# Optimization experiments

Hardware: AMD Instinct MI355X
Metric: run time of the kernel (lower is better)

The kernel has to match this reference:

```python
import jax, jax.numpy as jnp
import numpy as np

N, M = 65536, 512
CTRL = 128
IN_DIM = 128
READ_LEN = M + 6          # [M,1,1,3,1]
WRITE_LEN = 3 * M + 6     # [M,1,1,3,1,M,M]
EPS = 1e-16


def setup_inputs() -> dict:
    key = jax.random.key(0)
    ks = jax.random.split(key, 12)
    s = 0.02
    return {
        "x":   jax.random.normal(ks[0], (4, IN_DIM), jnp.float32),
        "mem": jax.random.normal(ks[1], (N, M), jnp.float32) * 0.05,
        "Wc":  jax.random.normal(ks[2], (CTRL, IN_DIM), jnp.float32) * s,
        "bc":  jnp.zeros((CTRL,), jnp.float32),
        "Wr":  jax.random.normal(ks[3], (READ_LEN, CTRL), jnp.float32) * s,
        "br":  jnp.zeros((READ_LEN,), jnp.float32),
        "Ww":  jax.random.normal(ks[4], (WRITE_LEN, CTRL), jnp.float32) * s,
        "bw":  jnp.zeros((WRITE_LEN,), jnp.float32),
        "W1":  jax.random.normal(ks[5], (200, M + CTRL), jnp.float32) * s,
        "b1":  jnp.zeros((200,), jnp.float32),
        "W2":  jax.random.normal(ks[6], (10, 200), jnp.float32) * s,
        "b2":  jnp.zeros((10,), jnp.float32),
    }


def _address(mem, k, beta, g, s, gamma, w_prev):
    # content + gate + circular shift + sharpen (standard NTM addressing)
    beta = jax.nn.softplus(beta)
    g = jax.nn.sigmoid(g)
    s = jax.nn.softmax(s)                      # (3,)
    gamma = 1.0 + jax.nn.softplus(gamma)
    # cosine similarity against all N memory rows
    dot = mem @ k                              # (N,)
    norms = jnp.sqrt(jnp.sum(mem * mem, axis=1)) * jnp.sqrt(jnp.sum(k * k)) + EPS
    wc = jax.nn.softmax(beta * dot / norms)    # content weights (N,)
    wg = g * wc + (1.0 - g) * w_prev           # gated
    # circular convolution with 3-tap shift kernel s = [s(-1), s(0), s(+1)]
    ws = s[0] * jnp.roll(wg, 1) + s[1] * wg + s[2] * jnp.roll(wg, -1)
    w = ws ** gamma                            # sharpen
    return w / (jnp.sum(w) + EPS)


def _forward(x, mem, Wc, bc, Wr, br, Ww, bw, W1, b1, W2, b2):
    cont = x @ Wc.T + bc                       # controller: (4, 128)
    w0 = jnp.full((N,), 1.0 / N, x.dtype)      # softmax of constant -> uniform

    def step(carry, c_t):
        mem, w_r, w_w = carry
        # ---- write head ----
        ow = c_t @ Ww.T + bw                   # (3M+6,)
        k, b, g, s, y = ow[:M], ow[M], ow[M+1], ow[M+2:M+5], ow[M+5]
        e, a = ow[M+6:2*M+6], ow[2*M+6:]
        w_w = _address(mem, k, b, g, s, y, w_w)
        e = jax.nn.sigmoid(e)
        mem = mem * (1.0 - jnp.outer(w_w, e)) + jnp.outer(w_w, a)
        # ---- read head ----
        orr = c_t @ Wr.T + br                  # (M+6,)
        k, b, g, s, y = orr[:M], orr[M], orr[M+1], orr[M+2:M+5], orr[M+5]
        w_r = _address(mem, k, b, g, s, y, w_r)
        r = w_r @ mem                          # (M,)
        # ---- output MLP ----
        h = jax.nn.relu(jnp.concatenate([c_t, r]) @ W1.T + b1)
        out = h @ W2.T + b2                    # (10,)
        return (mem, w_r, w_w), out

    _, outs = jax.lax.scan(step, (mem, w0, w0), cont)
    return outs                                # (4, 10)


def reference(x, mem, Wc, bc, Wr, br, Ww, bw, W1, b1, W2, b2):
    return _forward(x, mem, Wc, bc, Wr, br, Ww, bw, W1, b1, W2, b2)
```

## Files before the change

### kernel.cpp

```cpp
#include <hip/hip_runtime.h>
#include <hip/hip_cooperative_groups.h>
#include <hip/hip_fp16.h>
#include <math.h>

namespace cg = cooperative_groups;

#define NN    65536
#define CTRLD 128
#define WLEN  1542
#define RLEN  518
#define EPSF  1e-16f
#define GRIDB 1024
#define ROWSB 64
#define RPWV  16

struct KP {
  const float* mem0; const float* cont;
  float* mem16;
  const float* kW; const float* sW; const float* eW; const float* aW;
  const float* kR; const float* sR; float* kn;
  float *dotR, *dotW, *n2v;
  float *wunW, *pSW, *wunR, *pSR;
  float *pZr, *pZw;
  float *rp, *p2, *hbuf;
  const float *W1, *b1, *W2, *b2;
  float* out;
  const float *x, *Wc, *bc, *Ww, *bw, *Wr, *br;
  float *contw, *kWw, *sWw, *eWw, *aWw, *kRw, *sRw;
};

struct Smem { float red[256]; float big[2048]; float zsh[4][2]; };

__device__ __forceinline__ float softplusf_(float x){
    return x > 0.f ? x + log1pf(expf(-x)) : log1pf(expf(x));
}
__device__ __forceinline__ float sigmoidf_(float x){ return 1.f/(1.f+expf(-x)); }
__device__ __forceinline__ float dot4_(const float4& a, const float4& b){
    return a.x*b.x + a.y*b.y + a.z*b.z + a.w*b.w;
}

__device__ __forceinline__ float blockReduce256(float v, float* red){
    int t = threadIdx.x;
    red[t] = v; __syncthreads();
    for(int s = 128; s; s >>= 1){ if(t < s) red[t] += red[t+s]; __syncthreads(); }
    float r = red[0]; __syncthreads();
    return r;
}
__device__ __forceinline__ void waveReduce3(float& a, float& b, float& c){
    for(int o = 32; o; o >>= 1){
        a += __shfl_down(a,o); b += __shfl_down(b,o); c += __shfl_down(c,o);
    }
}
__device__ __forceinline__ void waveReduce1(float& a){
    for(int o = 32; o; o >>= 1) a += __shfl_down(a,o);
}

__device__ __forceinline__ void owor_phase(const KP& p, Smem& sm, int bid){
    float* cs = sm.big;
    int tid = threadIdx.x;
    for(int q = tid; q < 512; q += 256){
        int t = q >> 7, c = q & 127;
        float acc = p.bc[c];
        const float* xr = p.x + t*CTRLD;
        const float* wr = p.Wc + c*CTRLD;
        for(int d = 0; d < CTRLD; ++d) acc += xr[d]*wr[d];
        cs[q] = acc;
        if(bid == 0) p.contw[q] = acc;
    }
    __syncthreads();
    int idx = bid*256 + tid;
    if(idx < 4*WLEN){
        int t = idx / WLEN, o = idx % WLEN;
        float acc = p.bw[o];
        const float* cr = cs + t*CTRLD;
        const float* wr = p.Ww + o*CTRLD;
        for(int d = 0; d < CTRLD; ++d) acc += cr[d]*wr[d];
        if(o < 512)       p.kWw[t*512 + o] = acc;
        else if(o < 518)  p.sWw[t*8 + (o-512)] = acc;
        else if(o < 1030) p.eWw[t*512 + (o-518)] = sigmoidf_(acc);
        else              p.aWw[t*512 + (o-1030)] = acc;
    } else {
        int j = idx - 4*WLEN;
        if(j < 4*RLEN){
            int t = j / RLEN, o = j % RLEN;
            float acc = p.br[o];
            const float* cr = cs + t*CTRLD;
            const float* wr = p.Wr + o*CTRLD;
            for(int d = 0; d < CTRLD; ++d) acc += cr[d]*wr[d];
            if(o < 512) p.kRw[t*512 + o] = acc;
            else        p.sRw[t*8 + (o-512)] = acc;
        }
    }
    __syncthreads();
}

template<int CH, bool RP, bool UPD, bool DOTR, bool DOTW, bool CVT>
__device__ __forceinline__ void sweep_phase(const KP& p, Smem& sm, int rstep,
    const float* kRc, const float* sRc, int knRi,
    const float* kWn, const float* sWn, int knWi)
{
    constexpr int NW = CH + (UPD ? 1 : 0);
    constexpr int NA = (NW > 0) ? NW : 1;
    int t = threadIdx.x, bid = blockIdx.x;
    float wnorm[NA];
    #pragma unroll
    for(int j = 0; j < NW; ++j){
        float s = p.pSW[j*GRIDB+t] + p.pSW[j*GRIDB+t+256]
                + p.pSW[j*GRIDB+t+512] + p.pSW[j*GRIDB+t+768];
        wnorm[j] = 1.f/(blockReduce256(s, sm.red) + EPSF);
    }
    int wave = t >> 6, lane = t & 63;
    int c0 = 2*lane, c1 = 2*lane + 1;
    float4 ev0[NA], ev1[NA], av0[NA], av1[NA];
    #pragma unroll
    for(int j = 0; j < NW; ++j){
        ev0[j] = ((const float4*)(p.eW + j*512))[c0];
        ev1[j] = ((const float4*)(p.eW + j*512))[c1];
        av0[j] = ((const float4*)(p.aW + j*512))[c0];
        av1[j] = ((const float4*)(p.aW + j*512))[c1];
    }
    float4 kra, krb, kwa, kwb;
    float betaR = 0.f, betaW = 0.f, knRv = 1.f, knWv = 1.f;
    if constexpr(DOTR){
        kra = ((const float4*)kRc)[c0]; krb = ((const float4*)kRc)[c1];
        betaR = softplusf_(sRc[0]);
        float n2 = blockReduce256(dot4_(kra,kra) + dot4_(krb,krb), sm.red);
        knRv = sqrtf(n2*0.25f);
        if(t == 0 && bid == 0) p.kn[knRi] = knRv;
    }
    if constexpr(DOTW){
        kwa = ((const float4*)kWn)[c0]; kwb = ((const float4*)kWn)[c1];
        betaW = softplusf_(sWn[0]);
        float n2 = blockReduce256(dot4_(kwa,kwa) + dot4_(kwb,kwb), sm.red);
        knWv = sqrtf(n2*0.25f);
        if(t == 0 && bid == 0) p.kn[knWi] = knWv;
    }
    float4 rpA = {0,0,0,0}, rpB = {0,0,0,0};
    float zr = 0.f, zw = 0.f;
    int row0 = bid*ROWSB + wave*RPWV;
    for(int r = 0; r < RPWV; ++r){
        int row = row0 + r;
        float4 v0, v1;
        if constexpr(CVT){
            const float4* src = (const float4*)p.mem0;
            v0 = src[(size_t)row*128 + c0];
            v1 = src[(size_t)row*128 + c1];
        } else {
            float4 raw = ((const float4*)p.mem16)[(size_t)row*64 + lane];
            const __half2* hp = (const __half2*)&raw;
            float2 f0 = __half22float2(hp[0]);
            float2 f1 = __half22float2(hp[1]);
            float2 f2 = __half22float2(hp[2]);
            float2 f3 = __half22float2(hp[3]);
            v0 = make_float4(f0.x, f0.y, f1.x, f1.y);
            v1 = make_float4(f2.x, f2.y, f3.x, f3.y);
        }
        #pragma unroll
        for(int j = 0; j < CH; ++j){
            float w = p.wunW[(size_t)j*NN + row]*wnorm[j];
            v0.x = fmaf(w, fmaf(-ev0[j].x, v0.x, av0[j].x), v0.x);
            v0.y = fmaf(w, fmaf(-ev0[j].y, v0.y, av0[j].y), v0.y);
            v0.z = fmaf(w, fmaf(-ev0[j].z, v0.z, av0[j].z), v0.z);
            v0.w = fmaf(w, fmaf(-ev0[j].w, v0.w, av0[j].w), v0.w);
            v1.x = fmaf(w, fmaf(-ev1[j].x, v1.x, av1[j].x), v1.x);
            v1.y = fmaf(w, fmaf(-ev1[j].y, v1.y, av1[j].y), v1.y);
            v1.z = fmaf(w, fmaf(-ev1[j].z, v1.z, av1[j].z), v1.z);
            v1.w = fmaf(w, fmaf(-ev1[j].w, v1.w, av1[j].w), v1.w);
        }
        if constexpr(RP){
            float wr = p.wunR[(size_t)rstep*NN + row];
            rpA.x += wr*v0.x; rpA.y += wr*v0.y; rpA.z += wr*v0.z; rpA.w += wr*v0.w;
            rpB.x += wr*v1.x; rpB.y += wr*v1.y; rpB.z += wr*v1.z; rpB.w += wr*v1.w;
        }
        if constexpr(UPD){
            float w = p.wunW[(size_t)CH*NN + row]*wnorm[CH];
            v0.x = fmaf(w, fmaf(-ev0[CH].x, v0.x, av0[CH].x), v0.x);
            v0.y = fmaf(w, fmaf(-ev0[CH].y, v0.y, av0[CH].y), v0.y);
            v0.z = fmaf(w, fmaf(-ev0[CH].z, v0.z, av0[CH].z), v0.z);
            v0.w = fmaf(w, fmaf(-ev0[CH].w, v0.w, av0[CH].w), v0.w);
            v1.x = fmaf(w, fmaf(-ev1[CH].x, v1.x, av1[CH].x), v1.x);
            v1.y = fmaf(w, fmaf(-ev1[CH].y, v1.y, av1[CH].y), v1.y);
            v1.z = fmaf(w, fmaf(-ev1[CH].z, v1.z, av1[CH].z), v1.z);
            v1.w = fmaf(w, fmaf(-ev1[CH].w, v1.w, av1[CH].w), v1.w);
        }
        if constexpr(CVT){
            float4 packed;
            __half2* op = (__half2*)&packed;
            op[0] = __floats2half2_rn(v0.x, v0.y);
            op[1] = __floats2half2_rn(v0.z, v0.w);
            op[2] = __floats2half2_rn(v1.x, v1.y);
            op[3] = __floats2half2_rn(v1.z, v1.w);
            ((float4*)p.mem16)[(size_t)row*64 + lane] = packed;
        }
        if constexpr(DOTR || DOTW){
            float d = 0.f, dn = 0.f;
            float n = dot4_(v0,v0) + dot4_(v1,v1);
            if constexpr(DOTR) d  = dot4_(v0,kra) + dot4_(v1,krb);
            if constexpr(DOTW) dn = dot4_(v0,kwa) + dot4_(v1,kwb);
            waveReduce3(d, dn, n);
            if(lane == 0){
                p.n2v[row] = n;
                float sn = sqrtf(n);
                if constexpr(DOTR){ p.dotR[row] = d;  zr += expf(betaR*d /(sn*knRv + EPSF)); }
                if constexpr(DOTW){ p.dotW[row] = dn; zw += expf(betaW*dn/(sn*knWv + EPSF)); }
            }
        }
    }
    if constexpr(DOTR || DOTW){
        if(lane == 0){ sm.zsh[wave][0] = zr; sm.zsh[wave][1] = zw; }
    }
    if constexpr(RP){
        ((float4*)(sm.big + wave*512))[c0] = rpA;
        ((float4*)(sm.big + wave*512))[c1] = rpB;
    }
    __syncthreads();
    if constexpr(RP){
        p.rp[(size_t)bid*512 + t] =
            sm.big[t] + sm.big[512+t] + sm.big[1024+t] + sm.big[1536+t];
        p.rp[(size_t)bid*512 + t + 256] =
            sm.big[t+256] + sm.big[768+t] + sm.big[1280+t] + sm.big[1792+t];
    }
    if(t == 0){
        if constexpr(DOTR) p.pZr[bid] = sm.zsh[0][0]+sm.zsh[1][0]+sm.zsh[2][0]+sm.zsh[3][0];
        if constexpr(DOTW) p.pZw[bid] = sm.zsh[0][1]+sm.zsh[1][1]+sm.zsh[2][1]+sm.zsh[3][1];
    }
    __syncthreads();
}

__device__ __forceinline__ void whead_phase(const KP& p, Smem& sm,
    const float* sV, const float* dotv, const float* pZ,
    const float* wprev, const float* pSprev, int knidx,
    float* wun, float* pSout)
{
    int t = threadIdx.x, bid = blockIdx.x;
    float z = pZ[t] + pZ[t+256] + pZ[t+512] + pZ[t+768];
    float Z = blockReduce256(z, sm.red);
    float invSp = 1.f;
    if(pSprev){
        float sp = pSprev[t] + pSprev[t+256] + pSprev[t+512] + pSprev[t+768];
        invSp = 1.f/(blockReduce256(sp, sm.red) + EPSF);
    }
    float beta  = softplusf_(sV[0]);
    float g     = sigmoidf_(sV[1]);
    float s0 = sV[2], s1 = sV[3], s2 = sV[4];
    float smx = fmaxf(s0, fmaxf(s1, s2));
    float e0 = expf(s0-smx), e1 = expf(s1-smx), e2 = expf(s2-smx);
    float es = e0+e1+e2;
    s0 = e0/es; s1 = e1/es; s2 = e2/es;
    float gamma = 1.f + softplusf_(sV[5]);
    float knv = p.kn[knidx];
    float invZ = 1.f/Z;
    float wu = 0.f;
    if(t < ROWSB){
        int i = bid*ROWSB + t;
        int im = (i-1) & (NN-1), ip = (i+1) & (NN-1);
        auto wgf = [&](int j)->float{
            float a = beta*dotv[j]/(sqrtf(p.n2v[j])*knv + EPSF);
            float pv = wprev ? wprev[j]*invSp : (1.f/NN);
            return g*expf(a)*invZ + (1.f-g)*pv;
        };
        wu = powf(s0*wgf(im) + s1*wgf(i) + s2*wgf(ip), gamma);
        wun[i] = wu;
    }
    float S = blockReduce256(wu, sm.red);
    if(t == 0) pSout[bid] = S;
}

__device__ __forceinline__ void rsum1_phase(const KP& p, float* dst){
    int t = threadIdx.x, b = blockIdx.x;
    float2 acc; acc.x = 0.f; acc.y = 0.f;
    const float2* r2 = (const float2*)p.rp;
    for(int j = 0; j < 16; ++j){
        float2 v = r2[(size_t)(b*16 + j)*256 + t];
        acc.x += v.x; acc.y += v.y;
    }
    ((float2*)dst)[b*256 + t] = acc;
}

__device__ __forceinline__ void h_phase(const KP& p, Smem& sm, int hb, int step,
                                        const float* p2src){
    int t = threadIdx.x;
    const float* pS = p.pSR + step*GRIDB;
    float sp = pS[t] + pS[t+256] + pS[t+512] + pS[t+768];
    float invS = 1.f/(blockReduce256(sp, sm.red) + EPSF);
    float2 acc; acc.x = 0.f; acc.y = 0.f;
    const float2* q = (const float2*)p2src;
    for(int j = 0; j < 64; ++j){
        float2 v = q[j*256 + t];
        acc.x += v.x; acc.y += v.y;
    }
    float* conc = sm.big;
    conc[128 + 2*t]     = acc.x*invS;
    conc[128 + 2*t + 1] = acc.y*invS;
    if(t < 128) conc[t] = p.cont[step*128 + t];
    __syncthreads();
    int wave = t >> 6, lane = t & 63;
    for(int ol = wave; ol < 25; ol += 4){
        int o = hb*25 + ol;
        const float* wr = p.W1 + (size_t)o*640;
        float a = 0.f;
        for(int q2 = lane; q2 < 640; q2 += 64) a += wr[q2]*conc[q2];
        waveReduce1(a);
        if(lane == 0) p.hbuf[step*200 + o] = fmaxf(a + p.b1[o], 0.f);
    }
    __syncthreads();
}

__device__ __forceinline__ void out_phase(const KP& p, int step){
    int t = threadIdx.x;
    if(t < 10){
        float a = p.b2[t];
        const float* wr = p.W2 + t*200;
        const float* h = p.hbuf + step*200;
        for(int j = 0; j < 200; ++j) a += wr[j]*h[j];
        p.out[step*10 + t] = a;
    }
}

__device__ __forceinline__ void hfull_phase(const KP& p, Smem& sm, int step,
                                            const float* p2src){
    int t = threadIdx.x;
    const float* pS = p.pSR + step*GRIDB;
    float sp = pS[t] + pS[t+256] + pS[t+512] + pS[t+768];
    float invS = 1.f/(blockReduce256(sp, sm.red) + EPSF);
    float2 acc; acc.x = 0.f; acc.y = 0.f;
    const float2* q = (const float2*)p2src;
    for(int j = 0; j < 64; ++j){
        float2 v = q[j*256 + t];
        acc.x += v.x; acc.y += v.y;
    }
    float* conc = sm.big;
    conc[128 + 2*t]     = acc.x*invS;
    conc[128 + 2*t + 1] = acc.y*invS;
    if(t < 128) conc[t] = p.cont[step*128 + t];
    __syncthreads();
    int wave = t >> 6, lane = t & 63;
    float* hsh = sm.big + 1024;
    for(int o = wave; o < 200; o += 4){
        const float* wr = p.W1 + (size_t)o*640;
        float a = 0.f;
        for(int q2 = lane; q2 < 640; q2 += 64) a += wr[q2]*conc[q2];
        waveReduce1(a);
        if(lane == 0) hsh[o] = fmaxf(a + p.b1[o], 0.f);
    }
    __syncthreads();
    if(t < 10){
        float a = p.b2[t];
        const float* wr = p.W2 + t*200;
        for(int j = 0; j < 200; ++j) a += wr[j]*hsh[j];
        p.out[step*10 + t] = a;
    }
}

__global__ void __launch_bounds__(256, 4) k_coop(KP p){
    cg::grid_group g = cg::this_grid();
    __shared__ Smem sm;
    int bid = blockIdx.x;
    if(bid < 33) owor_phase(p, sm, bid);
    g.sync();
    sweep_phase<0,false,false,false,true,true>(p, sm, 0, nullptr,nullptr,0, p.kW, p.sW, 0);
    g.sync();
    whead_phase(p, sm, p.sW, p.dotW, p.pZw, nullptr, nullptr, 0, p.wunW, p.pSW);
    g.sync();
    sweep_phase<0,false,true,true,true,false>(p, sm, 0, p.kR, p.sR, 1, p.kW+512, p.sW+8, 2);
    g.sync();
    whead_phase(p, sm, p.sR, p.dotR, p.pZr, nullptr, nullptr, 1, p.wunR, p.pSR);
    whead_phase(p, sm, p.sW+8, p.dotW, p.pZw, p.wunW, p.pSW, 2, p.wunW+NN, p.pSW+GRIDB);
    g.sync();
    sweep_phase<1,true,true,true,true,false>(p, sm, 0, p.kR+512, p.sR+8, 3, p.kW+1024, p.sW+16, 4);
    g.sync();
    whead_phase(p, sm, p.sR+8, p.dotR, p.pZr, p.wunR, p.pSR, 3, p.wunR+NN, p.pSR+GRIDB);
    whead_phase(p, sm, p.sW+16, p.dotW, p.pZw, p.wunW+NN, p.pSW+GRIDB, 4,
                p.wunW+2*(size_t)NN, p.pSW+2*GRIDB);
    if(bid < 64) rsum1_phase(p, p.p2);
    g.sync();
    sweep_phase<2,true,true,true,true,false>(p, sm, 1, p.kR+1024, p.sR+16, 5, p.kW+1536, p.sW+24, 6);
    g.sync();
    whead_phase(p, sm, p.sR+16, p.dotR, p.pZr, p.wunR+NN, p.pSR+GRIDB, 5,
                p.wunR+2*(size_t)NN, p.pSR+2*GRIDB);
    whead_phase(p, sm, p.sW+24, p.dotW, p.pZw, p.wunW+2*(size_t)NN, p.pSW+2*GRIDB, 6,
                p.wunW+3*(size_t)NN, p.pSW+3*GRIDB);
    if(bid < 64) rsum1_phase(p, p.p2 + 64*512);
    if(bid >= 64 && bid < 72) h_phase(p, sm, bid-64, 0, p.p2);
    g.sync();
    sweep_phase<3,true,true,true,false,false>(p, sm, 2, p.kR+1536, p.sR+24, 7, nullptr,nullptr,0);
    g.sync();
    whead_phase(p, sm, p.sR+24, p.dotR, p.pZr, p.wunR+2*(size_t)NN, p.pSR+2*GRIDB, 7,
                p.wunR+3*(size_t)NN, p.pSR+3*GRIDB);
    if(bid < 64) rsum1_phase(p, p.p2);
    if(bid >= 64 && bid < 72) h_phase(p, sm, bid-64, 1, p.p2 + 64*512);
    if(bid == 72) out_phase(p, 0);
    g.sync();
    sweep_phase<4,true,false,false,false,false>(p, sm, 3, nullptr,nullptr,0, nullptr,nullptr,0);
    g.sync();
    if(bid < 64) rsum1_phase(p, p.p2 + 64*512);
    if(bid >= 64 && bid < 72) h_phase(p, sm, bid-64, 2, p.p2);
    if(bid == 72) out_phase(p, 1);
    g.sync();
    if(bid == 0) hfull_phase(p, sm, 3, p.p2 + 64*512);
    if(bid == 1) out_phase(p, 2);
}

__global__ void __launch_bounds__(256) g_owor(KP p){
    __shared__ Smem sm;
    owor_phase(p, sm, blockIdx.x);
}
__global__ void __launch_bounds__(256) g_sweepA(KP p){
    __shared__ Smem sm;
    sweep_phase<0,false,false,false,true,true>(p, sm, 0, nullptr,nullptr,0, p.kW, p.sW, 0);
}
__global__ void __launch_bounds__(256) g_sweepC0(KP p){
    __shared__ Smem sm;
    sweep_phase<0,false,true,true,true,false>(p, sm, 0, p.kR, p.sR, 1, p.kW+512, p.sW+8, 2);
}
__global__ void __launch_bounds__(256) g_sweepC1(KP p){
    __shared__ Smem sm;
    sweep_phase<1,true,true,true,true,false>(p, sm, 0, p.kR+512, p.sR+8, 3, p.kW+1024, p.sW+16, 4);
}
__global__ void __launch_bounds__(256) g_sweepC2(KP p){
    __shared__ Smem sm;
    sweep_phase<2,true,true,true,true,false>(p, sm, 1, p.kR+1024, p.sR+16, 5, p.kW+1536, p.sW+24, 6);
}
__global__ void __launch_bounds__(256) g_sweepC3(KP p){
    __shared__ Smem sm;
    sweep_phase<3,true,true,true,false,false>(p, sm, 2, p.kR+1536, p.sR+24, 7, nullptr,nullptr,0);
}
__global__ void __launch_bounds__(256) g_sweepC4(KP p){
    __shared__ Smem sm;
    sweep_phase<4,true,false,false,false,false>(p, sm, 3, nullptr,nullptr,0, nullptr,nullptr,0);
}
__global__ void __launch_bounds__(256) g_whead(KP p, const float* sV, const float* dotv,
    const float* pZ, const float* wprev, const float* pSprev, int knidx,
    float* wun, float* pSout){
    __shared__ Smem sm;
    whead_phase(p, sm, sV, dotv, pZ, wprev, pSprev, knidx, wun, pSout);
}
__global__ void __launch_bounds__(256) g_rsum1(KP p, float* dst){
    rsum1_phase(p, dst);
}
__global__ void __launch_bounds__(256) g_h(KP p, int step, const float* p2src){
    __shared__ Smem sm;
    h_phase(p, sm, blockIdx.x, step, p2src);
}
__global__ void __launch_bounds__(256) g_out(KP p, int step){
    out_phase(p, step);
}

extern "C" void kernel_launch(void* const* d_in, const int* in_sizes, int n_in,
                              void* d_out, int out_size, void* d_ws, size_t ws_size,
                              hipStream_t stream) {
    const float* x    = (const float*)d_in[0];
    const float* mem0 = (const float*)d_in[1];
    const float* Wc   = (const float*)d_in[2];
    const float* bc   = (const float*)d_in[3];
    const float* Wr   = (const float*)d_in[4];
    const float* br   = (const float*)d_in[5];
    const float* Ww   = (const float*)d_in[6];
    const float* bw   = (const float*)d_in[7];
    const float* W1   = (const float*)d_in[8];
    const float* b1   = (const float*)d_in[9];
    const float* W2   = (const float*)d_in[10];
    const float* b2   = (const float*)d_in[11];

    float* ws = (float*)d_ws;
    size_t off = 0;
    float* mem16 = ws + off; off += (size_t)NN*256;
    float* wunW = ws + off; off += 4*(size_t)NN;
    float* pSW  = ws + off; off += 4*GRIDB;
    float* wunR = ws + off; off += 4*(size_t)NN;
    float* pSR  = ws + off; off += 4*GRIDB;
    float* dotR = ws + off; off += NN;
    float* dotW = ws + off; off += NN;
    float* n2v  = ws + off; off += NN;
    float* pZr  = ws + off; off += GRIDB;
    float* pZw  = ws + off; off += GRIDB;
    float* cont = ws + off; off += 512;
    float* kW   = ws + off; off += 4*512;
    float* sW   = ws + off; off += 4*8;
    float* eW   = ws + off; off += 4*512;
    float* aW   = ws + off; off += 4*512;
    float* kR   = ws + off; off += 4*512;
    float* sR   = ws + off; off += 4*8;
    float* kn   = ws + off; off += 16;
    float* rp   = ws + off; off += (size_t)GRIDB*512;
    float* p2   = ws + off; off += 2*64*512;
    float* hbuf = ws + off; off += 1024;

    KP P;
    P.mem0 = mem0; P.cont = cont; P.mem16 = mem16;
    P.kW = kW; P.sW = sW; P.eW = eW; P.aW = aW; P.kR = kR; P.sR = sR; P.kn = kn;
    P.dotR = dotR; P.dotW = dotW; P.n2v = n2v;
    P.wunW = wunW; P.pSW = pSW; P.wunR = wunR; P.pSR = pSR;
    P.pZr = pZr; P.pZw = pZw;
    P.rp = rp; P.p2 = p2; P.hbuf = hbuf;
    P.W1 = W1; P.b1 = b1; P.W2 = W2; P.b2 = b2;
    P.out = (float*)d_out;
    P.x = x; P.Wc = Wc; P.bc = bc; P.Ww = Ww; P.bw = bw; P.Wr = Wr; P.br = br;
    P.contw = cont; P.kWw = kW; P.sWw = sW; P.eWw = eW; P.aWw = aW;
    P.kRw = kR; P.sRw = sR;

    bool useCoop = false;
    int coopAttr = 0;
    if(hipDeviceGetAttribute(&coopAttr, hipDeviceAttributeCooperativeLaunch, 0) == hipSuccess
       && coopAttr){
        int nCU = 0, maxb = 0;
        if(hipDeviceGetAttribute(&nCU, hipDeviceAttributeMultiprocessorCount, 0) == hipSuccess
           && hipOccupancyMaxActiveBlocksPerMultiprocessor(&maxb, k_coop, 256, 0) == hipSuccess
           && (long)maxb*(long)nCU >= GRIDB){
            useCoop = true;
        }
    }
    if(useCoop){
        void* args[] = { (void*)&P };
        hipError_t e = hipLaunchCooperativeKernel((const void*)k_coop,
                           dim3(GRIDB), dim3(256), args, 0, stream);
        if(e != hipSuccess){ (void)hipGetLastError(); useCoop = false; }
    }
    if(!useCoop){
        g_owor  <<<33, 256, 0, stream>>>(P);
        g_sweepA<<<GRIDB, 256, 0, stream>>>(P);
        g_whead <<<GRIDB, 256, 0, stream>>>(P, sW, dotW, pZw, nullptr, nullptr, 0, wunW, pSW);
        g_sweepC0<<<GRIDB, 256, 0, stream>>>(P);
        g_whead <<<GRIDB, 256, 0, stream>>>(P, sR, dotR, pZr, nullptr, nullptr, 1, wunR, pSR);
        g_whead <<<GRIDB, 256, 0, stream>>>(P, sW+8, dotW, pZw, wunW, pSW, 2, wunW+NN, pSW+GRIDB);
        g_sweepC1<<<GRIDB, 256, 0, stream>>>(P);
        g_whead <<<GRIDB, 256, 0, stream>>>(P, sR+8, dotR, pZr, wunR, pSR, 3, wunR+NN, pSR+GRIDB);
        g_whead <<<GRIDB, 256, 0, stream>>>(P, sW+16, dotW, pZw, wunW+NN, pSW+GRIDB, 4,
                                            wunW+2*(size_t)NN, pSW+2*GRIDB);
        g_rsum1 <<<64, 256, 0, stream>>>(P, p2);
        g_sweepC2<<<GRIDB, 256, 0, stream>>>(P);
        g_whead <<<GRIDB, 256, 0, stream>>>(P, sR+16, dotR, pZr, wunR+NN, pSR+GRIDB, 5,
                                            wunR+2*(size_t)NN, pSR+2*GRIDB);
        g_whead <<<GRIDB, 256, 0, stream>>>(P, sW+24, dotW, pZw, wunW+2*(size_t)NN, pSW+2*GRIDB, 6,
                                            wunW+3*(size_t)NN, pSW+3*GRIDB);
        g_rsum1 <<<64, 256, 0, stream>>>(P, p2 + 64*512);
        g_h     <<<8, 256, 0, stream>>>(P, 0, p2);
        g_sweepC3<<<GRIDB, 256, 0, stream>>>(P);
        g_whead <<<GRIDB, 256, 0, stream>>>(P, sR+24, dotR, pZr, wunR+2*(size_t)NN, pSR+2*GRIDB, 7,
                                            wunR+3*(size_t)NN, pSR+3*GRIDB);
        g_rsum1 <<<64, 256, 0, stream>>>(P, p2);
        g_h     <<<8, 256, 0, stream>>>(P, 1, p2 + 64*512);
        g_out   <<<1, 256, 0, stream>>>(P, 0);
        g_sweepC4<<<GRIDB, 256, 0, stream>>>(P);
        g_rsum1 <<<64, 256, 0, stream>>>(P, p2 + 64*512);
        g_h     <<<8, 256, 0, stream>>>(P, 2, p2);
        g_out   <<<1, 256, 0, stream>>>(P, 1);
        g_h     <<<8, 256, 0, stream>>>(P, 3, p2 + 64*512);
        g_out   <<<1, 256, 0, stream>>>(P, 2);
        g_out   <<<1, 256, 0, stream>>>(P, 3);
    }
    (void)in_sizes; (void)n_in; (void)out_size; (void)ws_size;
}
```

Baseline: 375.8 us.

## Store memory as scaled FP8 kept in LDS across cooperative sweep phases

Replaces the fp16 global copy of memory with FP8 (scaled by 64) and, in the cooperative kernel, keeps each block's 64-row slice resident in shared memory across all sweep phases, so the big matrix is re-read from LDS instead of HBM. Per-wave read partials are written straight to global memory without the in-block reduction, and the rsum pass now sums four times as many partials. This cuts HBM traffic but lowers precision to FP8, which risks accuracy failures. The larger LDS footprint may also reduce occupancy or break co-residency for the cooperative launch.

Result: no change. 381.5 us (+1.5%).

```diff
diff --git a/kernel.cpp b/kernel.cpp
--- a/kernel.cpp
+++ b/kernel.cpp
@@ -1,6 +1,5 @@
 #include <hip/hip_runtime.h>
 #include <hip/hip_cooperative_groups.h>
-#include <hip/hip_fp16.h>
 #include <math.h>
 
 namespace cg = cooperative_groups;
@@ -14,9 +13,11 @@
 #define ROWSB 64
 #define RPWV  16
 
+typedef float vf2 __attribute__((ext_vector_type(2)));
+
 struct KP {
   const float* mem0; const float* cont;
-  float* mem16;
+  unsigned* mem8;
   const float* kW; const float* sW; const float* eW; const float* aW;
   const float* kR; const float* sR; float* kn;
   float *dotR, *dotW, *n2v;
@@ -29,7 +30,12 @@
   float *contw, *kWw, *sWw, *eWw, *aWw, *kRw, *sRw;
 };
 
-struct Smem { float red[256]; float big[2048]; float zsh[4][2]; };
+struct SmemAll {
+  float red[256];
+  float big[1280];
+  float zsh[4][2];
+  unsigned m8[ROWSB*128];
+};
 
 __device__ __forceinline__ float softplusf_(float x){
     return x > 0.f ? x + log1pf(expf(-x)) : log1pf(expf(x));
@@ -55,7 +61,26 @@
     for(int o = 32; o; o >>= 1) a += __shfl_down(a,o);
 }
 
-__device__ __forceinline__ void owor_phase(const KP& p, Smem& sm, int bid){
+__device__ __forceinline__ void quant8(const float4& v0, const float4& v1,
+                                       unsigned& q0, unsigned& q1){
+    int a = __builtin_amdgcn_cvt_pk_fp8_f32(v0.x*64.f, v0.y*64.f, 0, false);
+    a     = __builtin_amdgcn_cvt_pk_fp8_f32(v0.z*64.f, v0.w*64.f, a, true);
+    int b = __builtin_amdgcn_cvt_pk_fp8_f32(v1.x*64.f, v1.y*64.f, 0, false);
+    b     = __builtin_amdgcn_cvt_pk_fp8_f32(v1.z*64.f, v1.w*64.f, b, true);
+    q0 = (unsigned)a; q1 = (unsigned)b;
+}
+__device__ __forceinline__ void dequant8(unsigned q0, unsigned q1,
+                                         float4& v0, float4& v1){
+    vf2 a = __builtin_amdgcn_cvt_pk_f32_fp8((int)q0, false);
+    vf2 b = __builtin_amdgcn_cvt_pk_f32_fp8((int)q0, true);
+    vf2 c = __builtin_amdgcn_cvt_pk_f32_fp8((int)q1, false);
+    vf2 d = __builtin_amdgcn_cvt_pk_f32_fp8((int)q1, true);
+    const float s = 1.f/64.f;
+    v0 = make_float4(a.x*s, a.y*s, b.x*s, b.y*s);
+    v1 = make_float4(c.x*s, c.y*s, d.x*s, d.y*s);
+}
+
+__device__ __forceinline__ void owor_phase(const KP& p, SmemAll& sm, int bid){
     float* cs = sm.big;
     int tid = threadIdx.x;
     for(int q = tid; q < 512; q += 256){
@@ -94,8 +119,8 @@
     __syncthreads();
 }
 
-template<int CH, bool RP, bool UPD, bool DOTR, bool DOTW, bool CVT>
-__device__ __forceinline__ void sweep_phase(const KP& p, Smem& sm, int rstep,
+template<int CH, bool RP, bool UPD, bool DOTR, bool DOTW, bool CVT, bool LDSM>
+__device__ __forceinline__ void sweep_phase(const KP& p, SmemAll& sm, int rstep,
     const float* kRc, const float* sRc, int knRi,
     const float* kWn, const float* sWn, int knWi)
 {
@@ -140,20 +165,22 @@
     int row0 = bid*ROWSB + wave*RPWV;
     for(int r = 0; r < RPWV; ++r){
         int row = row0 + r;
+        int lrow = wave*RPWV + r;
         float4 v0, v1;
         if constexpr(CVT){
             const float4* src = (const float4*)p.mem0;
             v0 = src[(size_t)row*128 + c0];
             v1 = src[(size_t)row*128 + c1];
         } else {
-            float4 raw = ((const float4*)p.mem16)[(size_t)row*64 + lane];
-            const __half2* hp = (const __half2*)&raw;
-            float2 f0 = __half22float2(hp[0]);
-            float2 f1 = __half22float2(hp[1]);
-            float2 f2 = __half22float2(hp[2]);
-            float2 f3 = __half22float2(hp[3]);
-            v0 = make_float4(f0.x, f0.y, f1.x, f1.y);
-            v1 = make_float4(f2.x, f2.y, f3.x, f3.y);
+            unsigned q0, q1;
+            if constexpr(LDSM){
+                q0 = sm.m8[lrow*128 + 2*lane];
+                q1 = sm.m8[lrow*128 + 2*lane + 1];
+            } else {
+                q0 = p.mem8[(size_t)row*128 + 2*lane];
+                q1 = p.mem8[(size_t)row*128 + 2*lane + 1];
+            }
+            dequant8(q0, q1, v0, v1);
         }
         #pragma unroll
         for(int j = 0; j < CH; ++j){
@@ -184,13 +211,15 @@
             v1.w = fmaf(w, fmaf(-ev1[CH].w, v1.w, av1[CH].w), v1.w);
         }
         if constexpr(CVT){
-            float4 packed;
-            __half2* op = (__half2*)&packed;
-            op[0] = __floats2half2_rn(v0.x, v0.y);
-            op[1] = __floats2half2_rn(v0.z, v0.w);
-            op[2] = __floats2half2_rn(v1.x, v1.y);
-            op[3] = __floats2half2_rn(v1.z, v1.w);
-            ((float4*)p.mem16)[(size_t)row*64 + lane] = packed;
+            unsigned q0, q1;
+            quant8(v0, v1, q0, q1);
+            if constexpr(LDSM){
+                sm.m8[lrow*128 + 2*lane]     = q0;
+                sm.m8[lrow*128 + 2*lane + 1] = q1;
+            } else {
+                p.mem8[(size_t)row*128 + 2*lane]     = q0;
+                p.mem8[(size_t)row*128 + 2*lane + 1] = q1;
+            }
         }
         if constexpr(DOTR || DOTW){
             float d = 0.f, dn = 0.f;
@@ -206,28 +235,23 @@
             }
         }
     }
+    if constexpr(RP){
+        float* dst = p.rp + ((size_t)(bid*4 + wave))*512;
+        ((float4*)dst)[c0] = rpA;
+        ((float4*)dst)[c1] = rpB;
+    }
     if constexpr(DOTR || DOTW){
         if(lane == 0){ sm.zsh[wave][0] = zr; sm.zsh[wave][1] = zw; }
-    }
-    if constexpr(RP){
-        ((float4*)(sm.big + wave*512))[c0] = rpA;
-        ((float4*)(sm.big + wave*512))[c1] = rpB;
-    }
-    __syncthreads();
-    if constexpr(RP){
-        p.rp[(size_t)bid*512 + t] =
-            sm.big[t] + sm.big[512+t] + sm.big[1024+t] + sm.big[1536+t];
-        p.rp[(size_t)bid*512 + t + 256] =
-            sm.big[t+256] + sm.big[768+t] + sm.big[1280+t] + sm.big[1792+t];
-    }
-    if(t == 0){
-        if constexpr(DOTR) p.pZr[bid] = sm.zsh[0][0]+sm.zsh[1][0]+sm.zsh[2][0]+sm.zsh[3][0];
-        if constexpr(DOTW) p.pZw[bid] = sm.zsh[0][1]+sm.zsh[1][1]+sm.zsh[2][1]+sm.zsh[3][1];
-    }
-    __syncthreads();
-}
-
-__device__ __forceinline__ void whead_phase(const KP& p, Smem& sm,
+        __syncthreads();
+        if(t == 0){
+            if constexpr(DOTR) p.pZr[bid] = sm.zsh[0][0]+sm.zsh[1][0]+sm.zsh[2][0]+sm.zsh[3][0];
+            if constexpr(DOTW) p.pZw[bid] = sm.zsh[0][1]+sm.zsh[1][1]+sm.zsh[2][1]+sm.zsh[3][1];
+        }
+    }
+    __syncthreads();
+}
+
+__device__ __forceinline__ void whead_phase(const KP& p, SmemAll& sm,
     const float* sV, const float* dotv, const float* pZ,
     const float* wprev, const float* pSprev, int knidx,
     float* wun, float* pSout)
@@ -270,14 +294,14 @@
     int t = threadIdx.x, b = blockIdx.x;
     float2 acc; acc.x = 0.f; acc.y = 0.f;
     const float2* r2 = (const float2*)p.rp;
-    for(int j = 0; j < 16; ++j){
-        float2 v = r2[(size_t)(b*16 + j)*256 + t];
+    for(int j = 0; j < 64; ++j){
+        float2 v = r2[(size_t)(b*64 + j)*256 + t];
         acc.x += v.x; acc.y += v.y;
     }
     ((float2*)dst)[b*256 + t] = acc;
 }
 
-__device__ __forceinline__ void h_phase(const KP& p, Smem& sm, int hb, int step,
+__device__ __forceinline__ void h_phase(const KP& p, SmemAll& sm, int hb, int step,
                                         const float* p2src){
     int t = threadIdx.x;
     const float* pS = p.pSR + step*GRIDB;
@@ -317,7 +341,7 @@
     }
 }
 
-__device__ __forceinline__ void hfull_phase(const KP& p, Smem& sm, int step,
+__device__ __forceinline__ void hfull_phase(const KP& p, SmemAll& sm, int step,
                                             const float* p2src){
     int t = threadIdx.x;
     const float* pS = p.pSR + step*GRIDB;
@@ -335,7 +359,7 @@
     if(t < 128) conc[t] = p.cont[step*128 + t];
     __syncthreads();
     int wave = t >> 6, lane = t & 63;
-    float* hsh = sm.big + 1024;
+    float* hsh = sm.big + 640;
     for(int o = wave; o < 200; o += 4){
         const float* wr = p.W1 + (size_t)o*640;
         float a = 0.f;
@@ -354,27 +378,27 @@
 
 __global__ void __launch_bounds__(256, 4) k_coop(KP p){
     cg::grid_group g = cg::this_grid();
-    __shared__ Smem sm;
+    __shared__ SmemAll sm;
     int bid = blockIdx.x;
     if(bid < 33) owor_phase(p, sm, bid);
     g.sync();
-    sweep_phase<0,false,false,false,true,true>(p, sm, 0, nullptr,nullptr,0, p.kW, p.sW, 0);
+    sweep_phase<0,false,false,false,true,true,true>(p, sm, 0, nullptr,nullptr,0, p.kW, p.sW, 0);
     g.sync();
     whead_phase(p, sm, p.sW, p.dotW, p.pZw, nullptr, nullptr, 0, p.wunW, p.pSW);
     g.sync();
-    sweep_phase<0,false,true,true,true,false>(p, sm, 0, p.kR, p.sR, 1, p.kW+512, p.sW+8, 2);
+    sweep_phase<0,false,true,true,true,false,true>(p, sm, 0, p.kR, p.sR, 1, p.kW+512, p.sW+8, 2);
     g.sync();
     whead_phase(p, sm, p.sR, p.dotR, p.pZr, nullptr, nullptr, 1, p.wunR, p.pSR);
     whead_phase(p, sm, p.sW+8, p.dotW, p.pZw, p.wunW, p.pSW, 2, p.wunW+NN, p.pSW+GRIDB);
     g.sync();
-    sweep_phase<1,true,true,true,true,false>(p, sm, 0, p.kR+512, p.sR+8, 3, p.kW+1024, p.sW+16, 4);
+    sweep_phase<1,true,true,true,true,false,true>(p, sm, 0, p.kR+512, p.sR+8, 3, p.kW+1024, p.sW+16, 4);
     g.sync();
     whead_phase(p, sm, p.sR+8, p.dotR, p.pZr, p.wunR, p.pSR, 3, p.wunR+NN, p.pSR+GRIDB);
     whead_phase(p, sm, p.sW+16, p.dotW, p.pZw, p.wunW+NN, p.pSW+GRIDB, 4,
                 p.wunW+2*(size_t)NN, p.pSW+2*GRIDB);
     if(bid < 64) rsum1_phase(p, p.p2);
     g.sync();
-    sweep_phase<2,true,true,true,true,false>(p, sm, 1, p.kR+1024, p.sR+16, 5, p.kW+1536, p.sW+24, 6);
+    sweep_phase<2,true,true,true,true,false,true>(p, sm, 1, p.kR+1024, p.sR+16, 5, p.kW+1536, p.sW+24, 6);
     g.sync();
     whead_phase(p, sm, p.sR+16, p.dotR, p.pZr, p.wunR+NN, p.pSR+GRIDB, 5,
                 p.wunR+2*(size_t)NN, p.pSR+2*GRIDB);
@@ -383,7 +407,7 @@
     if(bid < 64) rsum1_phase(p, p.p2 + 64*512);
     if(bid >= 64 && bid < 72) h_phase(p, sm, bid-64, 0, p.p2);
     g.sync();
-    sweep_phase<3,true,true,true,false,false>(p, sm, 2, p.kR+1536, p.sR+24, 7, nullptr,nullptr,0);
+    sweep_phase<3,true,true,true,false,false,true>(p, sm, 2, p.kR+1536, p.sR+24, 7, nullptr,nullptr,0);
     g.sync();
     whead_phase(p, sm, p.sR+24, p.dotR, p.pZr, p.wunR+2*(size_t)NN, p.pSR+2*GRIDB, 7,
                 p.wunR+3*(size_t)NN, p.pSR+3*GRIDB);
@@ -391,7 +415,7 @@
     if(bid >= 64 && bid < 72) h_phase(p, sm, bid-64, 1, p.p2 + 64*512);
     if(bid == 72) out_phase(p, 0);
     g.sync();
-    sweep_phase<4,true,false,false,false,false>(p, sm, 3, nullptr,nullptr,0, nullptr,nullptr,0);
+    sweep_phase<4,true,false,false,false,false,true>(p, sm, 3, nullptr,nullptr,0, nullptr,nullptr,0);
     g.sync();
     if(bid < 64) rsum1_phase(p, p.p2 + 64*512);
     if(bid >= 64 && bid < 72) h_phase(p, sm, bid-64, 2, p.p2);
@@ -402,44 +426,44 @@
 }
 
 __global__ void __launch_bounds__(256) g_owor(KP p){
-    __shared__ Smem sm;
+    __shared__ SmemAll sm;
     owor_phase(p, sm, blockIdx.x);
 }
 __global__ void __launch_bounds__(256) g_sweepA(KP p){
-    __shared__ Smem sm;
-    sweep_phase<0,false,false,false,true,true>(p, sm, 0, nullptr,nullptr,0, p.kW, p.sW, 0);
+    __shared__ SmemAll sm;
+    sweep_phase<0,false,false,false,true,true,false>(p, sm, 0, nullptr,nullptr,0, p.kW, p.sW, 0);
 }
 __global__ void __launch_bounds__(256) g_sweepC0(KP p){
-    __shared__ Smem sm;
-    sweep_phase<0,false,true,true,true,false>(p, sm, 0, p.kR, p.sR, 1, p.kW+512, p.sW+8, 2);
+    __shared__ SmemAll sm;
+    sweep_phase<0,false,true,true,true,false,false>(p, sm, 0, p.kR, p.sR, 1, p.kW+512, p.sW+8, 2);
 }
 __global__ void __launch_bounds__(256) g_sweepC1(KP p){
-    __shared__ Smem sm;
-    sweep_phase<1,true,true,true,true,false>(p, sm, 0, p.kR+512, p.sR+8, 3, p.kW+1024, p.sW+16, 4);
+    __shared__ SmemAll sm;
+    sweep_phase<1,true,true,true,true,false,false>(p, sm, 0, p.kR+512, p.sR+8, 3, p.kW+1024, p.sW+16, 4);
 }
 __global__ void __launch_bounds__(256) g_sweepC2(KP p){
-    __shared__ Smem sm;
-    sweep_phase<2,true,true,true,true,false>(p, sm, 1, p.kR+1024, p.sR+16, 5, p.kW+1536, p.sW+24, 6);
+    __shared__ SmemAll sm;
+    sweep_phase<2,true,true,true,true,false,false>(p, sm, 1, p.kR+1024, p.sR+16, 5, p.kW+1536, p.sW+24, 6);
 }
 __global__ void __launch_bounds__(256) g_sweepC3(KP p){
-    __shared__ Smem sm;
-    sweep_phase<3,true,true,true,false,false>(p, sm, 2, p.kR+1536, p.sR+24, 7, nullptr,nullptr,0);
+    __shared__ SmemAll sm;
+    sweep_phase<3,true,true,true,false,false,false>(p, sm, 2, p.kR+1536, p.sR+24, 7, nullptr,nullptr,0);
 }
 __global__ void __launch_bounds__(256) g_sweepC4(KP p){
-    __shared__ Smem sm;
-    sweep_phase<4,true,false,false,false,false>(p, sm, 3, nullptr,nullptr,0, nullptr,nullptr,0);
+    __shared__ SmemAll sm;
+    sweep_phase<4,true,false,false,false,false,false>(p, sm, 3, nullptr,nullptr,0, nullptr,nullptr,0);
 }
 __global__ void __launch_bounds__(256) g_whead(KP p, const float* sV, const float* dotv,
     const float* pZ, const float* wprev, const float* pSprev, int knidx,
     float* wun, float* pSout){
-    __shared__ Smem sm;
+    __shared__ SmemAll sm;
     whead_phase(p, sm, sV, dotv, pZ, wprev, pSprev, knidx, wun, pSout);
 }
 __global__ void __launch_bounds__(256) g_rsum1(KP p, float* dst){
     rsum1_phase(p, dst);
 }
 __global__ void __launch_bounds__(256) g_h(KP p, int step, const float* p2src){
-    __shared__ Smem sm;
+    __shared__ SmemAll sm;
     h_phase(p, sm, blockIdx.x, step, p2src);
 }
 __global__ void __launch_bounds__(256) g_out(KP p, int step){
@@ -464,7 +488,7 @@
 
     float* ws = (float*)d_ws;
     size_t off = 0;
-    float* mem16 = ws + off; off += (size_t)NN*256;
+    unsigned* mem8 = (unsigned*)(ws + off); off += (size_t)NN*128;
     float* wunW = ws + off; off += 4*(size_t)NN;
     float* pSW  = ws + off; off += 4*GRIDB;
     float* wunR = ws + off; off += 4*(size_t)NN;
@@ -482,12 +506,12 @@
     float* kR   = ws + off; off += 4*512;
     float* sR   = ws + off; off += 4*8;
     float* kn   = ws + off; off += 16;
-    float* rp   = ws + off; off += (size_t)GRIDB*512;
+    float* rp   = ws + off; off += (size_t)4*GRIDB*512;
     float* p2   = ws + off; off += 2*64*512;
     float* hbuf = ws + off; off += 1024;
 
     KP P;
-    P.mem0 = mem0; P.cont = cont; P.mem16 = mem16;
+    P.mem0 = mem0; P.cont = cont; P.mem8 = mem8;
     P.kW = kW; P.sW = sW; P.eW = eW; P.aW = aW; P.kR = kR; P.sR = sR; P.kn = kn;
     P.dotR = dotR; P.dotW = dotW; P.n2v = n2v;
     P.wunW = wunW; P.pSW = pSW; P.wunR = wunR; P.pSR = pSR;
```
